# Kernel optimization log

Hardware: AMD Instinct MI355X
Metric: run time of the kernel (lower is better)

Reference implementation:

```python
import math
import jax, jax.numpy as jnp
import numpy as np


def get_slopes(n):
    def pow2(n):
        start = 2.0 ** (-(2.0 ** (-(math.log2(n) - 3))))
        return [start * (start ** i) for i in range(n)]
    if math.log2(n).is_integer():
        return pow2(n)
    c = 2 ** math.floor(math.log2(n))
    return pow2(c) + get_slopes(2 * c)[0::2][: n - c]


def setup_inputs() -> dict:
    key = jax.random.key(0)
    B, T, C = 2, 2048, 1024
    ks = jax.random.split(key, 9)
    std = 0.02
    n_layers = 12
    inp = {
        "x": jax.random.normal(ks[0], (B, T, C), dtype=jnp.float32),
        # weights stored as [in, out] (transpose of torch Linear.weight)
        "Wq": std * jax.random.normal(ks[1], (C, C), dtype=jnp.float32),
        "bq": jnp.zeros((C,), dtype=jnp.float32),
        "Wk": std * jax.random.normal(ks[2], (C, C), dtype=jnp.float32),
        "bk": jnp.zeros((C,), dtype=jnp.float32),
        "Wv": std * jax.random.normal(ks[3], (C, C), dtype=jnp.float32),
        "bv": jnp.zeros((C,), dtype=jnp.float32),
        # fc_resid gets std 0.02/sqrt(2*num_layers)
        "Wo": (std / math.sqrt(2 * n_layers)) * jax.random.normal(ks[4], (C, C), dtype=jnp.float32),
        "bo": jnp.zeros((C,), dtype=jnp.float32),
        "n_head": 16,
    }
    return inp


def reference(x, Wq, bq, Wk, bk, Wv, bv, Wo, bo, n_head):
    B, T, C = x.shape
    hd = C // n_head
    # QKV projections, split heads: [B, nh, T, hd]
    def proj(W, b):
        return (x @ W + b).reshape(B, T, n_head, hd).transpose(0, 2, 1, 3)
    q, k, v = proj(Wq, bq), proj(Wk, bk), proj(Wv, bv)

    # ALiBi bias: bias[h, i, j] = -slope_h * (i - j) for j <= i, -inf above diag
    slopes = jnp.asarray(get_slopes(n_head), dtype=x.dtype)  # [nh]
    idx = jnp.arange(T)
    dist = (idx[:, None] - idx[None, :]).astype(x.dtype)  # [T, T], i - j
    bias = -slopes[:, None, None] * dist  # [nh, T, T]
    causal = idx[:, None] >= idx[None, :]
    bias = jnp.where(causal[None], bias, jnp.asarray(-jnp.inf, dtype=x.dtype))

    scale = 1.0 / math.sqrt(hd)
    scores = jnp.einsum("bnqh,bnkh->bnqk", q, k) * scale + bias[None]
    att = jax.nn.softmax(scores, axis=-1)
    y = jnp.einsum("bnqk,bnkh->bnqh", att, v)  # [B, nh, T, hd]
    y = y.transpose(0, 2, 1, 3).reshape(B, T, C)
    return y @ Wo + bo
```

## Files before the change

### kernel.cpp

```cpp
#include <hip/hip_runtime.h>


typedef unsigned short u16;
typedef unsigned int u32;
typedef __attribute__((ext_vector_type(8))) short bf16x8;
typedef __attribute__((ext_vector_type(4))) float f32x4;
typedef __attribute__((ext_vector_type(4))) unsigned short u16x4;

#define MFMA16x16(A, B, C_) __builtin_amdgcn_mfma_f32_16x16x32_bf16((A), (B), (C_), 0, 0, 0)

__device__ __forceinline__ u16 f2bf(float f) {
  u32 x = __builtin_bit_cast(u32, f);
  x += 0x7fff + ((x >> 16) & 1);
  return (u16)(x >> 16);
}

__device__ __forceinline__ void gload_lds16(const u16* g, u16* l) {
  __builtin_amdgcn_global_load_lds(
      (const __attribute__((address_space(1))) void*)g,
      (__attribute__((address_space(3))) void*)l, 16, 0, 0);
}

constexpr int T = 2048, C = 1024, HD = 64;
constexpr int BT = 2 * T;

__device__ __forceinline__ bf16x8 ldsfrag(const u16* lds, int row, int kchunk) {
  return *(const bf16x8*)(lds + row * 64 + (((kchunk) ^ (row & 7)) << 3));
}

__global__ __launch_bounds__(256) void convert_x_kernel(
    const float* __restrict__ xin, u16* __restrict__ xc) {
  int i = (blockIdx.x * 256 + threadIdx.x) * 8;
  const float4 a = *(const float4*)(xin + i);
  const float4 b = *(const float4*)(xin + i + 4);
  uint4 o;
  o.x = (u32)f2bf(a.x) | ((u32)f2bf(a.y) << 16);
  o.y = (u32)f2bf(a.z) | ((u32)f2bf(a.w) << 16);
  o.z = (u32)f2bf(b.x) | ((u32)f2bf(b.y) << 16);
  o.w = (u32)f2bf(b.z) | ((u32)f2bf(b.w) << 16);
  *(uint4*)(xc + i) = o;
}

__global__ __launch_bounds__(256) void transpose4_kernel(
    const float* __restrict__ w0, const float* __restrict__ w1,
    const float* __restrict__ w2, const float* __restrict__ w3,
    u16* __restrict__ wqkvT, u16* __restrict__ woT) {
  __shared__ u16 tile[32][33];
  const int z = blockIdx.z;
  const float* in = (z == 0) ? w0 : (z == 1) ? w1 : (z == 2) ? w2 : w3;
  u16* out = (z < 3) ? (wqkvT + (size_t)z * (1u << 20)) : woT;
  int tx = threadIdx.x, ty = threadIdx.y;
  int x = blockIdx.x * 32 + tx;
#pragma unroll
  for (int i = 0; i < 4; i++) {
    int y = blockIdx.y * 32 + ty + i * 8;
    tile[ty + i * 8][tx] = f2bf(in[y * 1024 + x]);
  }
  __syncthreads();
  int xo = blockIdx.y * 32 + tx;
#pragma unroll
  for (int i = 0; i < 4; i++) {
    int yo = blockIdx.x * 32 + ty + i * 8;
    out[yo * 1024 + xo] = tile[tx][ty + i * 8];
  }
}

template <int MODE>
__global__ __launch_bounds__(256) void gemm128_kernel(
    const u16* __restrict__ A, const u16* __restrict__ Bt,
    const float* __restrict__ b0, const float* __restrict__ b1,
    const float* __restrict__ b2,
    u16* __restrict__ qout, u16* __restrict__ kout, u16* __restrict__ vtout,
    float* __restrict__ fout) {
  constexpr int K = 1024;
  __shared__ __align__(16) u16 As[128 * 64];
  __shared__ __align__(16) u16 Bs[128 * 64];

  const int tid = threadIdx.x;
  const int w = tid >> 6, lane = tid & 63;
  const int l15 = lane & 15, quad = lane >> 4;
  const int m0 = blockIdx.y * 128, n0 = blockIdx.x * 128;
  const int wm = (w >> 1) * 64, wn = (w & 1) * 64;
  const int gsub = (lane & 7) ^ ((lane >> 3) & 7);
  const int rsub = lane >> 3;

  f32x4 acc[4][4] = {};

  const u16* Ag = A + (size_t)m0 * K;
  const u16* Bg = Bt + (size_t)n0 * K;

  for (int k0 = 0; k0 < K; k0 += 64) {
    __syncthreads();
#pragma unroll
    for (int t = 0; t < 4; t++) {
      int rbase = w * 32 + t * 8;
      gload_lds16(Ag + (size_t)(rbase + rsub) * K + k0 + gsub * 8, As + rbase * 64);
      gload_lds16(Bg + (size_t)(rbase + rsub) * K + k0 + gsub * 8, Bs + rbase * 64);
    }
    __syncthreads();
#pragma unroll
    for (int ks = 0; ks < 2; ks++) {
      bf16x8 af[4], bf[4];
#pragma unroll
      for (int mi = 0; mi < 4; mi++)
        af[mi] = ldsfrag(As, wm + mi * 16 + l15, (ks << 2) | quad);
#pragma unroll
      for (int ni = 0; ni < 4; ni++)
        bf[ni] = ldsfrag(Bs, wn + ni * 16 + l15, (ks << 2) | quad);
#pragma unroll
      for (int mi = 0; mi < 4; mi++)
#pragma unroll
        for (int ni = 0; ni < 4; ni++)
          acc[mi][ni] = MFMA16x16(af[mi], bf[ni], acc[mi][ni]);
    }
  }

  if constexpr (MODE == 0) {
    const int sel = n0 >> 10;
    const int nloc = n0 & 1023;
    if (sel < 2) {
      u16* D = (sel == 0) ? qout : kout;
      const float* bias = (sel == 0) ? b0 : b1;
#pragma unroll
      for (int mi = 0; mi < 4; mi++)
#pragma unroll
        for (int ni = 0; ni < 4; ni++) {
          int rb = m0 + wm + mi * 16 + quad * 4;
          int col = nloc + wn + ni * 16 + l15;
          float bb = bias[col];
#pragma unroll
          for (int r = 0; r < 4; r++)
            D[(size_t)(rb + r) * 1024 + col] = f2bf(acc[mi][ni][r] + bb);
        }
    } else {
#pragma unroll
      for (int mi = 0; mi < 4; mi++)
#pragma unroll
        for (int ni = 0; ni < 4; ni++) {
          int rb = m0 + wm + mi * 16 + quad * 4;
          int c = nloc + wn + ni * 16 + l15;
          float bb = b2[c];
          u16x4 pk;
#pragma unroll
          for (int r = 0; r < 4; r++) pk[r] = f2bf(acc[mi][ni][r] + bb);
          *(u16x4*)(vtout + (size_t)c * 4096 + rb) = pk;
        }
    }
  } else {
#pragma unroll
    for (int mi = 0; mi < 4; mi++)
#pragma unroll
      for (int ni = 0; ni < 4; ni++) {
        int rb = m0 + wm + mi * 16 + quad * 4;
        int col = n0 + wn + ni * 16 + l15;
        float bb = b0[col];
#pragma unroll
        for (int r = 0; r < 4; r++)
          fout[(size_t)(rb + r) * 1024 + col] = acc[mi][ni][r] + bb;
      }
  }
}

__global__ __launch_bounds__(256) void attn_kernel(
    const u16* __restrict__ qbuf, const u16* __restrict__ kbuf,
    const u16* __restrict__ vtbuf, u16* __restrict__ ybuf) {
  __shared__ __align__(16) u16 Qs[64 * 64];
  __shared__ __align__(16) u16 Ks[64 * 64];
  __shared__ __align__(16) u16 Vts[64 * 64];
  __shared__ __align__(16) u16 Ps[4][16 * 64];

  const int tid = threadIdx.x;
  const int w = tid >> 6, lane = tid & 63;
  const int l15 = lane & 15, quad = lane >> 4;
  const int bh = blockIdx.y, b = bh >> 4, h = bh & 15;
  const float slope = exp2f(-0.5f * (float)(h + 1));
  const float slope64 = slope * 64.f;
  const int gsub = (lane & 7) ^ ((lane >> 3) & 7);
  const int rsub = lane >> 3;

  const u16* kbase0 = kbuf + (size_t)b * T * C + h * HD;
  const u16* vtbase0 = vtbuf + (size_t)h * HD * BT + (size_t)b * T;
  u16* Pw = Ps[w];

#pragma unroll 1
  for (int half = 0; half < 2; half++) {
    const int qt = half == 0 ? (31 - (int)blockIdx.x) : (int)blockIdx.x;

    __syncthreads();
    const u16* qb = qbuf + (size_t)(b * T + qt * 64) * C + h * HD;
    {
      int rbase = w * 16;
      gload_lds16(qb + (size_t)(rbase + rsub) * C + gsub * 8, Qs + rbase * 64);
      gload_lds16(qb + (size_t)(rbase + 8 + rsub) * C + gsub * 8, Qs + (rbase + 8) * 64);
    }
    __syncthreads();
    bf16x8 aq0 = ldsfrag(Qs, w * 16 + l15, quad);
    bf16x8 aq1 = ldsfrag(Qs, w * 16 + l15, 4 + quad);

    f32x4 o[4] = {};
    float lsum[4] = {0.f, 0.f, 0.f, 0.f};
    float br[4][4];
#pragma unroll
    for (int ni = 0; ni < 4; ni++)
#pragma unroll
      for (int r = 0; r < 4; r++)
        br[ni][r] = slope * (float)(ni * 16 + l15 - qt * 64 - w * 16 - quad * 4 - r);

#pragma unroll 1
    for (int jt = 0; jt <= qt; jt++) {
      const u16* kb = kbase0 + (size_t)jt * 64 * C;
      const u16* vb = vtbase0 + jt * 64;
      __syncthreads();
      {
        int rbase = w * 16;
        gload_lds16(kb + (size_t)(rbase + rsub) * C + gsub * 8, Ks + rbase * 64);
        gload_lds16(kb + (size_t)(rbase + 8 + rsub) * C + gsub * 8, Ks + (rbase + 8) * 64);
        gload_lds16(vb + (size_t)(rbase + rsub) * BT + gsub * 8, Vts + rbase * 64);
        gload_lds16(vb + (size_t)(rbase + 8 + rsub) * BT + gsub * 8, Vts + (rbase + 8) * 64);
      }
      __syncthreads();

      f32x4 s[4];
#pragma unroll
      for (int ni = 0; ni < 4; ni++) {
        bf16x8 kf0 = ldsfrag(Ks, ni * 16 + l15, quad);
        bf16x8 kf1 = ldsfrag(Ks, ni * 16 + l15, 4 + quad);
        f32x4 z = {0.f, 0.f, 0.f, 0.f};
        z = MFMA16x16(aq0, kf0, z);
        z = MFMA16x16(aq1, kf1, z);
        s[ni] = z;
      }

      const bool diag = (jt == qt);
#pragma unroll
      for (int ni = 0; ni < 4; ni++)
#pragma unroll
        for (int r = 0; r < 4; r++) {
          float p = __expf(fmaf(s[ni][r], 0.125f, br[ni][r]));
          if (diag && (ni * 16 + l15) > (w * 16 + quad * 4 + r)) p = 0.f;
          lsum[r] += p;
          int prow = quad * 4 + r, pcol = ni * 16 + l15;
          Pw[prow * 64 + (((pcol >> 3) ^ (prow & 7)) << 3) + (pcol & 7)] = f2bf(p);
          br[ni][r] += slope64;
        }

      bf16x8 pa0 = ldsfrag(Pw, l15, quad);
      bf16x8 pa1 = ldsfrag(Pw, l15, 4 + quad);
#pragma unroll
      for (int ni = 0; ni < 4; ni++) {
        bf16x8 vf0 = ldsfrag(Vts, ni * 16 + l15, quad);
        bf16x8 vf1 = ldsfrag(Vts, ni * 16 + l15, 4 + quad);
        o[ni] = MFMA16x16(pa0, vf0, o[ni]);
        o[ni] = MFMA16x16(pa1, vf1, o[ni]);
      }
    }

#pragma unroll
    for (int r = 0; r < 4; r++) {
      float l = lsum[r];
      l += __shfl_xor(l, 1);
      l += __shfl_xor(l, 2);
      l += __shfl_xor(l, 4);
      l += __shfl_xor(l, 8);
      float inv = 1.f / l;
      int row_g = b * T + qt * 64 + w * 16 + quad * 4 + r;
      u16* yrow = ybuf + (size_t)row_g * C + h * HD;
#pragma unroll
      for (int ni = 0; ni < 4; ni++)
        yrow[ni * 16 + l15] = f2bf(o[ni][r] * inv);
    }
  }
}

extern "C" void kernel_launch(void* const* d_in, const int* in_sizes, int n_in,
                              void* d_out, int out_size, void* d_ws, size_t ws_size,
                              hipStream_t stream) {
  (void)in_sizes; (void)n_in; (void)out_size; (void)ws_size;
  const float* x  = (const float*)d_in[0];
  const float* Wq = (const float*)d_in[1];
  const float* bq = (const float*)d_in[2];
  const float* Wk = (const float*)d_in[3];
  const float* bk = (const float*)d_in[4];
  const float* Wv = (const float*)d_in[5];
  const float* bv = (const float*)d_in[6];
  const float* Wo = (const float*)d_in[7];
  const float* bo = (const float*)d_in[8];

  u16* ws = (u16*)d_ws;
  constexpr size_t M1 = 1u << 20;
  u16* wqkvT = ws;
  u16* woT   = ws + 3 * M1;
  u16* xc    = ws + 4 * M1;
  u16* qbuf  = ws + 8 * M1;
  u16* vtbuf = ws + 12 * M1;
  u16* kbuf  = (u16*)d_out;
  u16* ybuf  = qbuf;

  convert_x_kernel<<<2048, 256, 0, stream>>>(x, xc);
  transpose4_kernel<<<dim3(32, 32, 4), dim3(32, 8), 0, stream>>>(Wq, Wk, Wv, Wo, wqkvT, woT);
  gemm128_kernel<0><<<dim3(24, 32), 256, 0, stream>>>(
      xc, wqkvT, bq, bk, bv, qbuf, kbuf, vtbuf, nullptr);
  attn_kernel<<<dim3(16, 32), 256, 0, stream>>>(qbuf, kbuf, vtbuf, ybuf);
  gemm128_kernel<1><<<dim3(8, 32), 256, 0, stream>>>(
      ybuf, woT, bo, nullptr, nullptr, nullptr, nullptr, nullptr, (float*)d_out);
}
```

Baseline: 209.3 us.

## Split attention KV loop across two wave groups and narrow output GEMM tiles

```diff
diff --git a/kernel.cpp b/kernel.cpp
--- a/kernel.cpp
+++ b/kernel.cpp
@@ -65,13 +65,11 @@
   }
 }
 
-template <int MODE>
-__global__ __launch_bounds__(256) void gemm128_kernel(
+__global__ __launch_bounds__(256) void gemm_qkv_kernel(
     const u16* __restrict__ A, const u16* __restrict__ Bt,
     const float* __restrict__ b0, const float* __restrict__ b1,
     const float* __restrict__ b2,
-    u16* __restrict__ qout, u16* __restrict__ kout, u16* __restrict__ vtout,
-    float* __restrict__ fout) {
+    u16* __restrict__ qout, u16* __restrict__ kout, u16* __restrict__ vtout) {
   constexpr int K = 1024;
   __shared__ __align__(16) u16 As[128 * 64];
   __shared__ __align__(16) u16 Bs[128 * 64];
@@ -85,7 +83,6 @@
   const int rsub = lane >> 3;
 
   f32x4 acc[4][4] = {};
-
   const u16* Ag = A + (size_t)m0 * K;
   const u16* Bg = Bt + (size_t)n0 * K;
 
@@ -115,72 +112,124 @@
     }
   }
 
-  if constexpr (MODE == 0) {
-    const int sel = n0 >> 10;
-    const int nloc = n0 & 1023;
-    if (sel < 2) {
-      u16* D = (sel == 0) ? qout : kout;
-      const float* bias = (sel == 0) ? b0 : b1;
-#pragma unroll
-      for (int mi = 0; mi < 4; mi++)
-#pragma unroll
-        for (int ni = 0; ni < 4; ni++) {
-          int rb = m0 + wm + mi * 16 + quad * 4;
-          int col = nloc + wn + ni * 16 + l15;
-          float bb = bias[col];
-#pragma unroll
-          for (int r = 0; r < 4; r++)
-            D[(size_t)(rb + r) * 1024 + col] = f2bf(acc[mi][ni][r] + bb);
-        }
-    } else {
-#pragma unroll
-      for (int mi = 0; mi < 4; mi++)
-#pragma unroll
-        for (int ni = 0; ni < 4; ni++) {
-          int rb = m0 + wm + mi * 16 + quad * 4;
-          int c = nloc + wn + ni * 16 + l15;
-          float bb = b2[c];
-          u16x4 pk;
-#pragma unroll
-          for (int r = 0; r < 4; r++) pk[r] = f2bf(acc[mi][ni][r] + bb);
-          *(u16x4*)(vtout + (size_t)c * 4096 + rb) = pk;
-        }
-    }
-  } else {
+  const int sel = n0 >> 10;
+  const int nloc = n0 & 1023;
+  if (sel < 2) {
+    u16* D = (sel == 0) ? qout : kout;
+    const float* bias = (sel == 0) ? b0 : b1;
 #pragma unroll
     for (int mi = 0; mi < 4; mi++)
 #pragma unroll
       for (int ni = 0; ni < 4; ni++) {
         int rb = m0 + wm + mi * 16 + quad * 4;
-        int col = n0 + wn + ni * 16 + l15;
-        float bb = b0[col];
+        int col = nloc + wn + ni * 16 + l15;
+        float bb = bias[col];
 #pragma unroll
         for (int r = 0; r < 4; r++)
-          fout[(size_t)(rb + r) * 1024 + col] = acc[mi][ni][r] + bb;
-      }
-  }
-}
-
-__global__ __launch_bounds__(256) void attn_kernel(
+          D[(size_t)(rb + r) * 1024 + col] = f2bf(acc[mi][ni][r] + bb);
+      }
+  } else {
+#pragma unroll
+    for (int mi = 0; mi < 4; mi++)
+#pragma unroll
+      for (int ni = 0; ni < 4; ni++) {
+        int rb = m0 + wm + mi * 16 + quad * 4;
+        int c = nloc + wn + ni * 16 + l15;
+        float bb = b2[c];
+        u16x4 pk;
+#pragma unroll
+        for (int r = 0; r < 4; r++) pk[r] = f2bf(acc[mi][ni][r] + bb);
+        *(u16x4*)(vtout + (size_t)c * 4096 + rb) = pk;
+      }
+  }
+}
+
+__global__ __launch_bounds__(256) void gemm_out_kernel(
+    const u16* __restrict__ A, const u16* __restrict__ Bt,
+    const float* __restrict__ bias, float* __restrict__ fout) {
+  constexpr int K = 1024;
+  __shared__ __align__(16) u16 As[128 * 64];
+  __shared__ __align__(16) u16 Bs[64 * 64];
+
+  const int tid = threadIdx.x;
+  const int w = tid >> 6, lane = tid & 63;
+  const int l15 = lane & 15, quad = lane >> 4;
+  const int m0 = blockIdx.y * 128, n0 = blockIdx.x * 64;
+  const int wm = (w >> 1) * 64, wn = (w & 1) * 32;
+  const int gsub = (lane & 7) ^ ((lane >> 3) & 7);
+  const int rsub = lane >> 3;
+
+  f32x4 acc[4][2] = {};
+  const u16* Ag = A + (size_t)m0 * K;
+  const u16* Bg = Bt + (size_t)n0 * K;
+
+  for (int k0 = 0; k0 < K; k0 += 64) {
+    __syncthreads();
+#pragma unroll
+    for (int t = 0; t < 4; t++) {
+      int rbase = w * 32 + t * 8;
+      gload_lds16(Ag + (size_t)(rbase + rsub) * K + k0 + gsub * 8, As + rbase * 64);
+    }
+#pragma unroll
+    for (int t = 0; t < 2; t++) {
+      int rbase = w * 16 + t * 8;
+      gload_lds16(Bg + (size_t)(rbase + rsub) * K + k0 + gsub * 8, Bs + rbase * 64);
+    }
+    __syncthreads();
+#pragma unroll
+    for (int ks = 0; ks < 2; ks++) {
+      bf16x8 af[4], bf[2];
+#pragma unroll
+      for (int mi = 0; mi < 4; mi++)
+        af[mi] = ldsfrag(As, wm + mi * 16 + l15, (ks << 2) | quad);
+#pragma unroll
+      for (int ni = 0; ni < 2; ni++)
+        bf[ni] = ldsfrag(Bs, wn + ni * 16 + l15, (ks << 2) | quad);
+#pragma unroll
+      for (int mi = 0; mi < 4; mi++)
+#pragma unroll
+        for (int ni = 0; ni < 2; ni++)
+          acc[mi][ni] = MFMA16x16(af[mi], bf[ni], acc[mi][ni]);
+    }
+  }
+
+#pragma unroll
+  for (int mi = 0; mi < 4; mi++)
+#pragma unroll
+    for (int ni = 0; ni < 2; ni++) {
+      int rb = m0 + wm + mi * 16 + quad * 4;
+      int col = n0 + wn + ni * 16 + l15;
+      float bb = bias[col];
+#pragma unroll
+      for (int r = 0; r < 4; r++)
+        fout[(size_t)(rb + r) * 1024 + col] = acc[mi][ni][r] + bb;
+    }
+}
+
+__global__ __launch_bounds__(512, 4) void attn_kernel(
     const u16* __restrict__ qbuf, const u16* __restrict__ kbuf,
     const u16* __restrict__ vtbuf, u16* __restrict__ ybuf) {
   __shared__ __align__(16) u16 Qs[64 * 64];
-  __shared__ __align__(16) u16 Ks[64 * 64];
-  __shared__ __align__(16) u16 Vts[64 * 64];
-  __shared__ __align__(16) u16 Ps[4][16 * 64];
+  __shared__ __align__(16) u16 KVs[4][64 * 64];
+  __shared__ __align__(16) u16 Ps[8][16 * 64];
 
   const int tid = threadIdx.x;
   const int w = tid >> 6, lane = tid & 63;
+  const int wq = w & 3, g = w >> 2;
   const int l15 = lane & 15, quad = lane >> 4;
   const int bh = blockIdx.y, b = bh >> 4, h = bh & 15;
   const float slope = exp2f(-0.5f * (float)(h + 1));
-  const float slope64 = slope * 64.f;
+  const float slope128 = slope * 128.f;
   const int gsub = (lane & 7) ^ ((lane >> 3) & 7);
   const int rsub = lane >> 3;
 
   const u16* kbase0 = kbuf + (size_t)b * T * C + h * HD;
   const u16* vtbase0 = vtbuf + (size_t)h * HD * BT + (size_t)b * T;
   u16* Pw = Ps[w];
+  const int st = w >> 1;
+  const int skind = st & 1;
+  const int sjt = st >> 1;
+  const int srb = (w & 1) * 32;
 
 #pragma unroll 1
   for (int half = 0; half < 2; half++) {
@@ -188,86 +237,113 @@
 
     __syncthreads();
     const u16* qb = qbuf + (size_t)(b * T + qt * 64) * C + h * HD;
-    {
-      int rbase = w * 16;
-      gload_lds16(qb + (size_t)(rbase + rsub) * C + gsub * 8, Qs + rbase * 64);
-      gload_lds16(qb + (size_t)(rbase + 8 + rsub) * C + gsub * 8, Qs + (rbase + 8) * 64);
-    }
-    __syncthreads();
-    bf16x8 aq0 = ldsfrag(Qs, w * 16 + l15, quad);
-    bf16x8 aq1 = ldsfrag(Qs, w * 16 + l15, 4 + quad);
+    gload_lds16(qb + (size_t)(w * 8 + rsub) * C + gsub * 8, Qs + (w * 8) * 64);
+    __syncthreads();
+    bf16x8 aq0 = ldsfrag(Qs, wq * 16 + l15, quad);
+    bf16x8 aq1 = ldsfrag(Qs, wq * 16 + l15, 4 + quad);
 
     f32x4 o[4] = {};
     float lsum[4] = {0.f, 0.f, 0.f, 0.f};
     float br[4][4];
+    const int ig0 = qt * 64 + wq * 16 + quad * 4;
 #pragma unroll
     for (int ni = 0; ni < 4; ni++)
 #pragma unroll
       for (int r = 0; r < 4; r++)
-        br[ni][r] = slope * (float)(ni * 16 + l15 - qt * 64 - w * 16 - quad * 4 - r);
-
+        br[ni][r] = slope * (float)(g * 64 + ni * 16 + l15 - ig0 - r);
+
+    const int iters = (qt + 2) >> 1;
 #pragma unroll 1
-    for (int jt = 0; jt <= qt; jt++) {
-      const u16* kb = kbase0 + (size_t)jt * 64 * C;
-      const u16* vb = vtbase0 + jt * 64;
+    for (int it = 0; it < iters; it++) {
       __syncthreads();
       {
-        int rbase = w * 16;
-        gload_lds16(kb + (size_t)(rbase + rsub) * C + gsub * 8, Ks + rbase * 64);
-        gload_lds16(kb + (size_t)(rbase + 8 + rsub) * C + gsub * 8, Ks + (rbase + 8) * 64);
-        gload_lds16(vb + (size_t)(rbase + rsub) * BT + gsub * 8, Vts + rbase * 64);
-        gload_lds16(vb + (size_t)(rbase + 8 + rsub) * BT + gsub * 8, Vts + (rbase + 8) * 64);
+        int jtv = 2 * it + sjt;
+        int jtr = jtv > qt ? qt : jtv;
+        const u16* base = skind ? (vtbase0 + jtr * 64)
+                                : (kbase0 + (size_t)jtr * 64 * C);
+        const int stride = skind ? BT : C;
+        u16* dst = KVs[skind * 2 + sjt] + srb * 64;
+#pragma unroll
+        for (int c2 = 0; c2 < 4; c2++)
+          gload_lds16(base + (size_t)(srb + c2 * 8 + rsub) * stride + gsub * 8,
+                      dst + c2 * 8 * 64);
       }
       __syncthreads();
 
+      const int jtv = 2 * it + g;
+      const u16* Kw = KVs[g];
+      const u16* Vw = KVs[2 + g];
+
       f32x4 s[4];
 #pragma unroll
       for (int ni = 0; ni < 4; ni++) {
-        bf16x8 kf0 = ldsfrag(Ks, ni * 16 + l15, quad);
-        bf16x8 kf1 = ldsfrag(Ks, ni * 16 + l15, 4 + quad);
+        bf16x8 kf0 = ldsfrag(Kw, ni * 16 + l15, quad);
+        bf16x8 kf1 = ldsfrag(Kw, ni * 16 + l15, 4 + quad);
         f32x4 z = {0.f, 0.f, 0.f, 0.f};
         z = MFMA16x16(aq0, kf0, z);
         z = MFMA16x16(aq1, kf1, z);
         s[ni] = z;
       }
 
-      const bool diag = (jt == qt);
+      const bool edge = (jtv >= qt);
 #pragma unroll
       for (int ni = 0; ni < 4; ni++)
 #pragma unroll
         for (int r = 0; r < 4; r++) {
           float p = __expf(fmaf(s[ni][r], 0.125f, br[ni][r]));
-          if (diag && (ni * 16 + l15) > (w * 16 + quad * 4 + r)) p = 0.f;
+          if (edge && (jtv * 64 + ni * 16 + l15) > (ig0 + r)) p = 0.f;
           lsum[r] += p;
           int prow = quad * 4 + r, pcol = ni * 16 + l15;
           Pw[prow * 64 + (((pcol >> 3) ^ (prow & 7)) << 3) + (pcol & 7)] = f2bf(p);
-          br[ni][r] += slope64;
+          br[ni][r] += slope128;
         }
 
       bf16x8 pa0 = ldsfrag(Pw, l15, quad);
       bf16x8 pa1 = ldsfrag(Pw, l15, 4 + quad);
 #pragma unroll
       for (int ni = 0; ni < 4; ni++) {
-        bf16x8 vf0 = ldsfrag(Vts, ni * 16 + l15, quad);
-        bf16x8 vf1 = ldsfrag(Vts, ni * 16 + l15, 4 + quad);
+        bf16x8 vf0 = ldsfrag(Vw, ni * 16 + l15, quad);
+        bf16x8 vf1 = ldsfrag(Vw, ni * 16 + l15, 4 + quad);
         o[ni] = MFMA16x16(pa0, vf0, o[ni]);
         o[ni] = MFMA16x16(pa1, vf1, o[ni]);
       }
     }
 
-#pragma unroll
-    for (int r = 0; r < 4; r++) {
-      float l = lsum[r];
-      l += __shfl_xor(l, 1);
-      l += __shfl_xor(l, 2);
-      l += __shfl_xor(l, 4);
-      l += __shfl_xor(l, 8);
-      float inv = 1.f / l;
-      int row_g = b * T + qt * 64 + w * 16 + quad * 4 + r;
-      u16* yrow = ybuf + (size_t)row_g * C + h * HD;
+    __syncthreads();
+    float* sc = (float*)KVs;
+    float* Osc = sc + wq * 1024;
+    float* Lsc = sc + 4096 + wq * 256;
+    if (g == 1) {
 #pragma unroll
       for (int ni = 0; ni < 4; ni++)
-        yrow[ni * 16 + l15] = f2bf(o[ni][r] * inv);
+#pragma unroll
+        for (int r = 0; r < 4; r++)
+          Osc[(quad * 4 + r) * 64 + ni * 16 + l15] = o[ni][r];
+#pragma unroll
+      for (int r = 0; r < 4; r++)
+        Lsc[(quad * 4 + r) * 16 + l15] = lsum[r];
+    }
+    __syncthreads();
+    if (g == 0) {
+#pragma unroll
+      for (int ni = 0; ni < 4; ni++)
+#pragma unroll
+        for (int r = 0; r < 4; r++)
+          o[ni][r] += Osc[(quad * 4 + r) * 64 + ni * 16 + l15];
+#pragma unroll
+      for (int r = 0; r < 4; r++) {
+        float l = lsum[r] + Lsc[(quad * 4 + r) * 16 + l15];
+        l += __shfl_xor(l, 1);
+        l += __shfl_xor(l, 2);
+        l += __shfl_xor(l, 4);
+        l += __shfl_xor(l, 8);
+        float inv = 1.f / l;
+        int row_g = b * T + qt * 64 + wq * 16 + quad * 4 + r;
+        u16* yrow = ybuf + (size_t)row_g * C + h * HD;
+#pragma unroll
+        for (int ni = 0; ni < 4; ni++)
+          yrow[ni * 16 + l15] = f2bf(o[ni][r] * inv);
+      }
     }
   }
 }
@@ -298,9 +374,8 @@
 
   convert_x_kernel<<<2048, 256, 0, stream>>>(x, xc);
   transpose4_kernel<<<dim3(32, 32, 4), dim3(32, 8), 0, stream>>>(Wq, Wk, Wv, Wo, wqkvT, woT);
-  gemm128_kernel<0><<<dim3(24, 32), 256, 0, stream>>>(
-      xc, wqkvT, bq, bk, bv, qbuf, kbuf, vtbuf, nullptr);
-  attn_kernel<<<dim3(16, 32), 256, 0, stream>>>(qbuf, kbuf, vtbuf, ybuf);
-  gemm128_kernel<1><<<dim3(8, 32), 256, 0, stream>>>(
-      ybuf, woT, bo, nullptr, nullptr, nullptr, nullptr, nullptr, (float*)d_out);
-}
+  gemm_qkv_kernel<<<dim3(24, 32), 256, 0, stream>>>(
+      xc, wqkvT, bq, bk, bv, qbuf, kbuf, vtbuf);
+  attn_kernel<<<dim3(16, 32), 512, 0, stream>>>(qbuf, kbuf, vtbuf, ybuf);
+  gemm_out_kernel<<<dim3(16, 32), 256, 0, stream>>>(ybuf, woT, bo, (float*)d_out);
+}
```

Result: faster. 199.3 us (-4.8%).
